# Kernel tuning notes

Measured on AMD Instinct MI355X. Metric: run time of the kernel, lower is better.

The kernel has to match this reference:

```python
import jax, jax.numpy as jnp
import numpy as np

DIM = 1024
NUM_HEADS = 16
HEAD_DIM = DIM // NUM_HEADS


def setup_inputs() -> dict:
    key = jax.random.key(0)
    k_x, k_qkv, k_proj, k_pb = jax.random.split(key, 4)
    B, N, C = 4, 2048, DIM
    x = jax.random.normal(k_x, (B, N, C), dtype=jnp.float32)
    # Dense 'qkv': kernel [C, 3C], no bias (qkv_bias=False)
    W_qkv = jax.random.normal(k_qkv, (C, 3 * C), dtype=jnp.float32) * (C ** -0.5)
    # Dense 'proj': kernel [C, C] + bias [C] (proj_bias=True)
    W_proj = jax.random.normal(k_proj, (C, C), dtype=jnp.float32) * (C ** -0.5)
    b_proj = jax.random.normal(k_pb, (C,), dtype=jnp.float32) * 0.01
    return {"x": x, "W_qkv": W_qkv, "W_proj": W_proj, "b_proj": b_proj}


def reference(x, W_qkv, W_proj, b_proj):
    B, N, C = x.shape
    H, D = NUM_HEADS, HEAD_DIM
    scale = D ** -0.5
    qkv = x @ W_qkv  # [B, N, 3C]
    qkv = qkv.reshape(B, N, 3, H, D).transpose(2, 0, 3, 1, 4)  # [3, B, H, N, D]
    q, k, v = qkv[0], qkv[1], qkv[2]
    attn = jnp.einsum('bhnd,bhmd->bhnm', q, k) * scale  # [B, H, N, N]
    attn = jax.nn.softmax(attn, axis=-1)
    out = jnp.einsum('bhnm,bhmd->bhnd', attn, v)  # [B, H, N, D]
    out = out.transpose(0, 2, 1, 3).reshape(B, N, C)
    return out @ W_proj + b_proj
```

## Files before the change

### kernel.cpp

```cpp
#include <hip/hip_runtime.h>
#include <hip/hip_bf16.h>
#include <cstdint>
#include <cstddef>

#define C_DIM 1024
#define N_HEADS 16
#define H_DIM 64
#define N_BATCH 4
#define SEQ_LEN 2048
#define N_BH 64
#define M_ROWS 8192

typedef __attribute__((ext_vector_type(8))) short bf16x8;
typedef __attribute__((ext_vector_type(4))) float f32x4;
typedef __attribute__((ext_vector_type(8))) float f32x8;
typedef __attribute__((ext_vector_type(2))) float f32x2;
typedef __attribute__((ext_vector_type(16))) float f32x16;
typedef __attribute__((ext_vector_type(4))) unsigned short us4;
typedef __attribute__((ext_vector_type(8))) unsigned short us8;
typedef __attribute__((ext_vector_type(4))) float fl4;

__device__ __forceinline__ unsigned short f2bf(float f) {
  union { float f; unsigned u; } v; v.f = f;
  unsigned r = (v.u + 0x7FFFu + ((v.u >> 16) & 1u)) >> 16;
  return (unsigned short)r;
}

__device__ __forceinline__ unsigned pk2(float a, float b) {
  union { __hip_bfloat162 h2; unsigned u; } c;
  c.h2 = __float22bfloat162_rn(float2{a, b});
  return c.u;
}

__device__ __forceinline__ void gload16(const void* g, void* l) {
  __builtin_amdgcn_global_load_lds(
      (const __attribute__((address_space(1))) unsigned int*)g,
      (__attribute__((address_space(3))) unsigned int*)l, 16, 0, 0);
}

__global__ void cast_x_kernel(const float* __restrict__ in,
                              unsigned short* __restrict__ out, int n8) {
  int i = blockIdx.x * blockDim.x + threadIdx.x;
  if (i >= n8) return;
  const fl4* p = reinterpret_cast<const fl4*>(in) + (size_t)i * 2;
  fl4 a = p[0], b = p[1];
  us8 w;
  w[0] = f2bf(a[0]); w[1] = f2bf(a[1]); w[2] = f2bf(a[2]); w[3] = f2bf(a[3]);
  w[4] = f2bf(b[0]); w[5] = f2bf(b[1]); w[6] = f2bf(b[2]); w[7] = f2bf(b[3]);
  *(reinterpret_cast<us8*>(out) + i) = w;
}

__global__ void transpose_cast_kernel(const float* __restrict__ in,
                                      unsigned short* __restrict__ out,
                                      int R, int C) {
  __shared__ float tile[64][65];
  int t = threadIdx.x;
  int tc = blockIdx.x * 64;
  int tr = blockIdx.y * 64;
  int hi = t >> 4, lo = t & 15;
#pragma unroll
  for (int i = 0; i < 4; ++i) {
    int r = i * 16 + hi;
    int c = lo * 4;
    fl4 v = *reinterpret_cast<const fl4*>(&in[(size_t)(tr + r) * C + tc + c]);
    tile[c + 0][r] = v[0]; tile[c + 1][r] = v[1];
    tile[c + 2][r] = v[2]; tile[c + 3][r] = v[3];
  }
  __syncthreads();
#pragma unroll
  for (int i = 0; i < 4; ++i) {
    int c = i * 16 + hi;
    int r = lo * 4;
    us4 w;
    w[0] = f2bf(tile[c][r + 0]); w[1] = f2bf(tile[c][r + 1]);
    w[2] = f2bf(tile[c][r + 2]); w[3] = f2bf(tile[c][r + 3]);
    *reinterpret_cast<us4*>(&out[(size_t)(tc + c) * R + tr + r]) = w;
  }
}

__global__ void transpose_v_kernel(const unsigned short* __restrict__ V,
                                   unsigned short* __restrict__ Vt) {
  __shared__ unsigned short tile[64][72];
  int t = threadIdx.x;
  int bh = blockIdx.y;
  int n0 = blockIdx.x * 64;
  const unsigned short* src = V + ((size_t)bh * SEQ_LEN + n0) * H_DIM;
#pragma unroll
  for (int i = 0; i < 2; ++i) {
    int c = t + i * 256;
    int r = c >> 3;
    int col = (c & 7) * 8;
    us8 v = *reinterpret_cast<const us8*>(&src[r * H_DIM + col]);
#pragma unroll
    for (int j = 0; j < 8; ++j) tile[col + j][r] = v[j];
  }
  __syncthreads();
  unsigned short* dst = Vt + (size_t)bh * H_DIM * SEQ_LEN + n0;
#pragma unroll
  for (int i = 0; i < 2; ++i) {
    int c = t + i * 256;
    int d = c >> 3;
    int col = (c & 7) * 8;
    us8 w;
#pragma unroll
    for (int j = 0; j < 8; ++j) w[j] = tile[d][col + j];
    *reinterpret_cast<us8*>(&dst[(size_t)d * SEQ_LEN + col]) = w;
  }
}

template <int EPI>
__global__ __launch_bounds__(256) void gemm_bt_kernel(
    const unsigned short* __restrict__ A, const unsigned short* __restrict__ Bt,
    unsigned short* __restrict__ outQ, unsigned short* __restrict__ outK,
    unsigned short* __restrict__ outV, float* __restrict__ outF,
    const float* __restrict__ bias, int K) {
  __shared__ unsigned short Alds[128 * 32];
  __shared__ unsigned short Blds[128 * 32];
  int tid = threadIdx.x;
  int lane = tid & 63, wave = tid >> 6;
  int wr = wave >> 1, wc = wave & 1;
  int brow = blockIdx.y * 128;
  int bcol = blockIdx.x * 128;
  int rr = lane & 15, g8 = (lane >> 4) * 8;

  f32x4 acc[4][4];
#pragma unroll
  for (int m = 0; m < 4; ++m)
#pragma unroll
    for (int n = 0; n < 4; ++n) acc[m][n] = (f32x4){0.f, 0.f, 0.f, 0.f};

  int c0 = tid, c1 = tid + 256;
  int r0 = c0 >> 2, o0 = (c0 & 3) * 8;
  int r1 = c1 >> 2, o1 = (c1 & 3) * 8;
  const unsigned short* Ar0 = A + (size_t)(brow + r0) * K + o0;
  const unsigned short* Ar1 = A + (size_t)(brow + r1) * K + o1;
  const unsigned short* Br0 = Bt + (size_t)(bcol + r0) * K + o0;
  const unsigned short* Br1 = Bt + (size_t)(bcol + r1) * K + o1;

  for (int k0 = 0; k0 < K; k0 += 32) {
    __syncthreads();
    gload16(Ar0 + k0, &Alds[c0 * 8]);
    gload16(Ar1 + k0, &Alds[c1 * 8]);
    gload16(Br0 + k0, &Blds[c0 * 8]);
    gload16(Br1 + k0, &Blds[c1 * 8]);
    __syncthreads();
    bf16x8 af[4], bf[4];
#pragma unroll
    for (int m = 0; m < 4; ++m)
      af[m] = *reinterpret_cast<const bf16x8*>(
          &Alds[(wr * 64 + m * 16 + rr) * 32 + g8]);
#pragma unroll
    for (int n = 0; n < 4; ++n)
      bf[n] = *reinterpret_cast<const bf16x8*>(
          &Blds[(wc * 64 + n * 16 + rr) * 32 + g8]);
#pragma unroll
    for (int m = 0; m < 4; ++m)
#pragma unroll
      for (int n = 0; n < 4; ++n)
        acc[m][n] = __builtin_amdgcn_mfma_f32_16x16x32_bf16(af[m], bf[n],
                                                            acc[m][n], 0, 0, 0);
  }

  if (EPI == 0) {
    int part = bcol >> 10;
#pragma unroll
    for (int n = 0; n < 4; ++n) {
      int col = (bcol & 1023) + wc * 64 + n * 16 + rr;
      int h = col >> 6, d = col & 63;
#pragma unroll
      for (int m = 0; m < 4; ++m) {
        int rowb = brow + wr * 64 + m * 16 + (lane >> 4) * 4;
#pragma unroll
        for (int r = 0; r < 4; ++r) {
          int mr = rowb + r;
          int b = mr >> 11, nr = mr & 2047;
          size_t idx = ((size_t)((b * N_HEADS + h) * SEQ_LEN + nr)) * H_DIM + d;
          float v = acc[m][n][r];
          if (part == 0)
            outQ[idx] = f2bf(v * 0.1803368801111837f);
          else if (part == 1)
            outK[idx] = f2bf(v);
          else
            outV[idx] = f2bf(v);
        }
      }
    }
  } else {
#pragma unroll
    for (int n = 0; n < 4; ++n) {
      int col = bcol + wc * 64 + n * 16 + rr;
      float bv = bias[col];
#pragma unroll
      for (int m = 0; m < 4; ++m) {
        int rowb = brow + wr * 64 + m * 16 + (lane >> 4) * 4;
#pragma unroll
        for (int r = 0; r < 4; ++r)
          outF[(size_t)(rowb + r) * C_DIM + col] = acc[m][n][r] + bv;
      }
    }
  }
}

__global__ __launch_bounds__(256) void attn_kernel(
    const unsigned short* __restrict__ Qs, const unsigned short* __restrict__ Ks,
    const unsigned short* __restrict__ Vts, unsigned short* __restrict__ Oo) {
  __shared__ __attribute__((aligned(16))) char lds[32768];
  const int tid = threadIdx.x;
  const int lane = tid & 63, wave = tid >> 6;
  const int l31 = lane & 31, h5 = lane >> 5;
  int i = blockIdx.x;
  int bh = (i & 7) * 8 + ((i >> 3) & 7);
  int qb = i >> 6;
  const int q0 = qb * 128 + wave * 32;
  const int bb = bh >> 4, hh = bh & 15;

  const unsigned short* Qb = Qs + (size_t)bh * SEQ_LEN * H_DIM;
  const char* Kg = (const char*)(Ks + (size_t)bh * SEQ_LEN * H_DIM);
  const char* Vg = (const char*)(Vts + (size_t)bh * H_DIM * SEQ_LEN);

  bf16x8 qf[4];
#pragma unroll
  for (int ks = 0; ks < 4; ++ks)
    qf[ks] = *reinterpret_cast<const bf16x8*>(
        &Qb[(size_t)(q0 + l31) * H_DIM + ks * 16 + h5 * 8]);

  int kaddr[4];
  int r7 = (l31 & 7) << 4;
#pragma unroll
  for (int ks = 0; ks < 4; ++ks)
    kaddr[ks] = l31 * 128 + ((ks * 32 + h5 * 16) ^ r7);
  int vaddr[2][2][2];
#pragma unroll
  for (int dt = 0; dt < 2; ++dt) {
    int d = dt * 32 + l31;
    int sw = (d & 7) << 4;
#pragma unroll
    for (int s = 0; s < 2; ++s)
#pragma unroll
      for (int m = 0; m < 2; ++m)
        vaddr[dt][s][m] = 8192 + d * 128 + ((s * 64 + m * 32 + h5 * 16) ^ sw);
  }

  const int rowc = lane >> 3;
  const int scb = (((lane & 7) ^ rowc)) * 16;
  const char* gK0 = Kg + (size_t)(wave * 16 + rowc) * 128 + scb;
  const char* gK1 = gK0 + 8 * 128;
  const char* gV0 = Vg + (size_t)(wave * 16 + rowc) * 4096 + scb;
  const char* gV1 = gV0 + 8 * 4096;
  char* lK0 = lds + wave * 2048 + (lane & 63) * 16;
  char* lV0 = lds + 8192 + wave * 2048 + (lane & 63) * 16;

  f32x16 oacc[2];
#pragma unroll
  for (int dt = 0; dt < 2; ++dt)
#pragma unroll
    for (int r = 0; r < 16; ++r) oacc[dt][r] = 0.f;
  float lsum = 0.f;

  f32x16 z16;
#pragma unroll
  for (int r = 0; r < 16; ++r) z16[r] = 0.f;

  {
    gload16(gK0, lK0);
    gload16(gK1, lK0 + 1024);
    gload16(gV0, lV0);
    gload16(gV1, lV0 + 1024);
  }
  __syncthreads();

#pragma unroll 2
  for (int t = 0; t < 32; ++t) {
    int boff = (t & 1) * 16384;
    if (t < 31) {
      int nb = ((t + 1) & 1) * 16384;
      size_t kR = (size_t)(t + 1) * 64 * 128;
      size_t kV = (size_t)(t + 1) * 128;
      gload16(gK0 + kR, lK0 + nb);
      gload16(gK1 + kR, lK0 + nb + 1024);
      gload16(gV0 + kV, lV0 + nb);
      gload16(gV1 + kV, lV0 + nb + 1024);
    }
#pragma unroll
    for (int s = 0; s < 2; ++s) {
      bf16x8 kf[4];
#pragma unroll
      for (int ks = 0; ks < 4; ++ks)
        kf[ks] = *reinterpret_cast<const bf16x8*>(
            lds + boff + kaddr[ks] + s * 4096);
      __builtin_amdgcn_s_setprio(1);
      f32x16 sa = __builtin_amdgcn_mfma_f32_32x32x16_bf16(kf[0], qf[0], z16,
                                                          0, 0, 0);
#pragma unroll
      for (int ks = 1; ks < 4; ++ks)
        sa = __builtin_amdgcn_mfma_f32_32x32x16_bf16(kf[ks], qf[ks], sa, 0, 0, 0);
      __builtin_amdgcn_s_setprio(0);
      f32x16 pv;
#pragma unroll
      for (int r = 0; r < 16; ++r) pv[r] = __builtin_amdgcn_exp2f(sa[r]);
      {
        f32x8 h8 = __builtin_shufflevector(pv, pv, 0, 1, 2, 3, 4, 5, 6, 7) +
                   __builtin_shufflevector(pv, pv, 8, 9, 10, 11, 12, 13, 14, 15);
        f32x4 h4 = __builtin_shufflevector(h8, h8, 0, 1, 2, 3) +
                   __builtin_shufflevector(h8, h8, 4, 5, 6, 7);
        f32x2 h2 = __builtin_shufflevector(h4, h4, 0, 1) +
                   __builtin_shufflevector(h4, h4, 2, 3);
        lsum += h2[0] + h2[1];
      }
      unsigned X0 = pk2(pv[0], pv[1]), X1 = pk2(pv[2], pv[3]);
      unsigned X2 = pk2(pv[4], pv[5]), X3 = pk2(pv[6], pv[7]);
      unsigned X4 = pk2(pv[8], pv[9]), X5 = pk2(pv[10], pv[11]);
      unsigned X6 = pk2(pv[12], pv[13]), X7 = pk2(pv[14], pv[15]);
      asm("v_permlane32_swap_b32 %0, %1" : "+v"(X0), "+v"(X2));
      asm("v_permlane32_swap_b32 %0, %1" : "+v"(X1), "+v"(X3));
      asm("v_permlane32_swap_b32 %0, %1" : "+v"(X4), "+v"(X6));
      asm("v_permlane32_swap_b32 %0, %1" : "+v"(X5), "+v"(X7));
      union { unsigned u[4]; bf16x8 v; } pf0, pf1;
      pf0.u[0] = X0; pf0.u[1] = X1; pf0.u[2] = X2; pf0.u[3] = X3;
      pf1.u[0] = X4; pf1.u[1] = X5; pf1.u[2] = X6; pf1.u[3] = X7;
      bf16x8 vf[2][2];
#pragma unroll
      for (int dt = 0; dt < 2; ++dt)
#pragma unroll
        for (int m = 0; m < 2; ++m)
          vf[dt][m] = *reinterpret_cast<const bf16x8*>(
              lds + boff + vaddr[dt][s][m]);
      __builtin_amdgcn_s_setprio(1);
#pragma unroll
      for (int dt = 0; dt < 2; ++dt) {
        oacc[dt] = __builtin_amdgcn_mfma_f32_32x32x16_bf16(vf[dt][0], pf0.v,
                                                           oacc[dt], 0, 0, 0);
        oacc[dt] = __builtin_amdgcn_mfma_f32_32x32x16_bf16(vf[dt][1], pf1.v,
                                                           oacc[dt], 0, 0, 0);
      }
      __builtin_amdgcn_s_setprio(0);
    }
    __syncthreads();
  }

  lsum += __shfl_xor(lsum, 32);
  float inv = 1.f / lsum;
  int n = q0 + l31;
  unsigned short* orow = Oo + ((size_t)bb * SEQ_LEN + n) * C_DIM + hh * H_DIM;
#pragma unroll
  for (int dt = 0; dt < 2; ++dt)
#pragma unroll
    for (int G = 0; G < 4; ++G) {
      us4 w;
#pragma unroll
      for (int u = 0; u < 4; ++u) w[u] = f2bf(oacc[dt][G * 4 + u] * inv);
      *reinterpret_cast<us4*>(&orow[dt * 32 + G * 8 + h5 * 4]) = w;
    }
}

extern "C" void kernel_launch(void* const* d_in, const int* in_sizes, int n_in,
                              void* d_out, int out_size, void* d_ws,
                              size_t ws_size, hipStream_t stream) {
  const float* x = (const float*)d_in[0];
  const float* Wqkv = (const float*)d_in[1];
  const float* Wproj = (const float*)d_in[2];
  const float* bproj = (const float*)d_in[3];
  float* out = (float*)d_out;

  unsigned short* xbf = (unsigned short*)d_ws;
  unsigned short* Wtqkv = xbf + (size_t)M_ROWS * C_DIM;
  unsigned short* Wtproj = Wtqkv + (size_t)3 * C_DIM * C_DIM;
  unsigned short* Qb = Wtproj + (size_t)C_DIM * C_DIM;
  unsigned short* Kb = Qb + (size_t)N_BH * SEQ_LEN * H_DIM;
  unsigned short* Vb = Kb + (size_t)N_BH * SEQ_LEN * H_DIM;
  unsigned short* Vtb = Vb + (size_t)N_BH * SEQ_LEN * H_DIM;
  unsigned short* Ob = Vb;

  cast_x_kernel<<<4096, 256, 0, stream>>>(x, xbf, M_ROWS * C_DIM / 8);
  transpose_cast_kernel<<<dim3(48, 16), 256, 0, stream>>>(Wqkv, Wtqkv, C_DIM,
                                                          3 * C_DIM);
  transpose_cast_kernel<<<dim3(16, 16), 256, 0, stream>>>(Wproj, Wtproj, C_DIM,
                                                          C_DIM);
  gemm_bt_kernel<0><<<dim3(24, 64), 256, 0, stream>>>(
      xbf, Wtqkv, Qb, Kb, Vb, nullptr, nullptr, C_DIM);
  transpose_v_kernel<<<dim3(32, 64), 256, 0, stream>>>(Vb, Vtb);
  attn_kernel<<<dim3(1024), 256, 0, stream>>>(Qb, Kb, Vtb, Ob);
  gemm_bt_kernel<1><<<dim3(8, 64), 256, 0, stream>>>(
      Ob, Wtproj, nullptr, nullptr, nullptr, out, bproj, C_DIM);
}
```

Baseline: 227.6 us.

## Triple-buffer GEMM with swizzled LDS and fuse V transpose into QKV epilogue

Rewrites the GEMM main loop to use a 3-stage LDS ring buffer with async global-to-LDS loads issued two tiles ahead, a single barrier per k-step, XOR-swizzled LDS layout to avoid bank conflicts, and raised wave priority around the MFMA block. The QKV epilogue now writes V directly in transposed layout, removing the separate transpose_v kernel and its extra pass over V. It also reuses the x buffer for the attention output. This trades more LDS per block (48KB) for fewer stalls and one fewer launch, with risk of lower occupancy and uncoalesced scattered Vt stores.

```diff
diff --git a/kernel.cpp b/kernel.cpp
--- a/kernel.cpp
+++ b/kernel.cpp
@@ -78,50 +78,36 @@
   }
 }
 
-__global__ void transpose_v_kernel(const unsigned short* __restrict__ V,
-                                   unsigned short* __restrict__ Vt) {
-  __shared__ unsigned short tile[64][72];
-  int t = threadIdx.x;
-  int bh = blockIdx.y;
-  int n0 = blockIdx.x * 64;
-  const unsigned short* src = V + ((size_t)bh * SEQ_LEN + n0) * H_DIM;
-#pragma unroll
-  for (int i = 0; i < 2; ++i) {
-    int c = t + i * 256;
-    int r = c >> 3;
-    int col = (c & 7) * 8;
-    us8 v = *reinterpret_cast<const us8*>(&src[r * H_DIM + col]);
-#pragma unroll
-    for (int j = 0; j < 8; ++j) tile[col + j][r] = v[j];
-  }
-  __syncthreads();
-  unsigned short* dst = Vt + (size_t)bh * H_DIM * SEQ_LEN + n0;
-#pragma unroll
-  for (int i = 0; i < 2; ++i) {
-    int c = t + i * 256;
-    int d = c >> 3;
-    int col = (c & 7) * 8;
-    us8 w;
-#pragma unroll
-    for (int j = 0; j < 8; ++j) w[j] = tile[d][col + j];
-    *reinterpret_cast<us8*>(&dst[(size_t)d * SEQ_LEN + col]) = w;
-  }
-}
-
 template <int EPI>
-__global__ __launch_bounds__(256) void gemm_bt_kernel(
+__global__ __launch_bounds__(256, 3) void gemm_v2_kernel(
     const unsigned short* __restrict__ A, const unsigned short* __restrict__ Bt,
     unsigned short* __restrict__ outQ, unsigned short* __restrict__ outK,
-    unsigned short* __restrict__ outV, float* __restrict__ outF,
+    unsigned short* __restrict__ outVt, float* __restrict__ outF,
     const float* __restrict__ bias, int K) {
-  __shared__ unsigned short Alds[128 * 32];
-  __shared__ unsigned short Blds[128 * 32];
-  int tid = threadIdx.x;
-  int lane = tid & 63, wave = tid >> 6;
-  int wr = wave >> 1, wc = wave & 1;
-  int brow = blockIdx.y * 128;
-  int bcol = blockIdx.x * 128;
-  int rr = lane & 15, g8 = (lane >> 4) * 8;
+  __shared__ __attribute__((aligned(16))) char lds[3 * 16384];
+  const int tid = threadIdx.x;
+  const int lane = tid & 63, wave = tid >> 6;
+  const int wr = wave >> 1, wn = wave & 1;
+  const int brow = blockIdx.y * 128;
+  const int bcol = blockIdx.x * 128;
+  const int rr = lane & 15, g = lane >> 4;
+
+  const int rbase =
+      (rr >> 1) * 128 + (((((rr & 1) << 2) | g) ^ (rr >> 1)) << 4);
+
+  const int s1 = tid + 256;
+  const int l0 = tid >> 3, v0 = (tid & 7) ^ (l0 & 7);
+  const int l1 = s1 >> 3, v1 = (s1 & 7) ^ (l1 & 7);
+  const int m0 = 2 * l0 + (v0 >> 2), g0 = v0 & 3;
+  const int m1 = 2 * l1 + (v1 >> 2), g1 = v1 & 3;
+  const char* srcA0 = (const char*)(A + (size_t)(brow + m0) * K + g0 * 8);
+  const char* srcA1 = (const char*)(A + (size_t)(brow + m1) * K + g1 * 8);
+  const char* srcB0 = (const char*)(Bt + (size_t)(bcol + m0) * K + g0 * 8);
+  const char* srcB1 = (const char*)(Bt + (size_t)(bcol + m1) * K + g1 * 8);
+  const int oA0 = wave * 1024 + (lane & 63) * 16;
+  const int oA1 = oA0 + 4096;
+  const int oB0 = oA0 + 8192;
+  const int oB1 = oA0 + 12288;
 
   f32x4 acc[4][4];
 #pragma unroll
@@ -129,73 +115,102 @@
 #pragma unroll
     for (int n = 0; n < 4; ++n) acc[m][n] = (f32x4){0.f, 0.f, 0.f, 0.f};
 
-  int c0 = tid, c1 = tid + 256;
-  int r0 = c0 >> 2, o0 = (c0 & 3) * 8;
-  int r1 = c1 >> 2, o1 = (c1 & 3) * 8;
-  const unsigned short* Ar0 = A + (size_t)(brow + r0) * K + o0;
-  const unsigned short* Ar1 = A + (size_t)(brow + r1) * K + o1;
-  const unsigned short* Br0 = Bt + (size_t)(bcol + r0) * K + o0;
-  const unsigned short* Br1 = Bt + (size_t)(bcol + r1) * K + o1;
-
-  for (int k0 = 0; k0 < K; k0 += 32) {
-    __syncthreads();
-    gload16(Ar0 + k0, &Alds[c0 * 8]);
-    gload16(Ar1 + k0, &Alds[c1 * 8]);
-    gload16(Br0 + k0, &Blds[c0 * 8]);
-    gload16(Br1 + k0, &Blds[c1 * 8]);
-    __syncthreads();
+  const int NT = K >> 5;
+
+#pragma unroll
+  for (int pt = 0; pt < 2; ++pt) {
+    char* bb = lds + pt * 16384;
+    size_t ko = (size_t)pt * 64;
+    gload16(srcA0 + ko, bb + oA0);
+    gload16(srcA1 + ko, bb + oA1);
+    gload16(srcB0 + ko, bb + oB0);
+    gload16(srcB1 + ko, bb + oB1);
+  }
+
+  int rbuf = 0, nbuf = 2;
+  for (int kt = 0; kt < NT; ++kt) {
+    if (kt < NT - 1) {
+      asm volatile("s_waitcnt vmcnt(4)" ::: "memory");
+    } else {
+      asm volatile("s_waitcnt vmcnt(0)" ::: "memory");
+    }
+    __builtin_amdgcn_sched_barrier(0);
+    __builtin_amdgcn_s_barrier();
+    __builtin_amdgcn_sched_barrier(0);
+    if (kt + 2 < NT) {
+      char* bb = lds + nbuf * 16384;
+      size_t ko = (size_t)(kt + 2) * 64;
+      gload16(srcA0 + ko, bb + oA0);
+      gload16(srcA1 + ko, bb + oA1);
+      gload16(srcB0 + ko, bb + oB0);
+      gload16(srcB1 + ko, bb + oB1);
+    }
+    const char* rb = lds + rbuf * 16384;
     bf16x8 af[4], bf[4];
 #pragma unroll
-    for (int m = 0; m < 4; ++m)
-      af[m] = *reinterpret_cast<const bf16x8*>(
-          &Alds[(wr * 64 + m * 16 + rr) * 32 + g8]);
-#pragma unroll
-    for (int n = 0; n < 4; ++n)
-      bf[n] = *reinterpret_cast<const bf16x8*>(
-          &Blds[(wc * 64 + n * 16 + rr) * 32 + g8]);
-#pragma unroll
-    for (int m = 0; m < 4; ++m)
-#pragma unroll
-      for (int n = 0; n < 4; ++n)
-        acc[m][n] = __builtin_amdgcn_mfma_f32_16x16x32_bf16(af[m], bf[n],
-                                                            acc[m][n], 0, 0, 0);
+    for (int fm = 0; fm < 4; ++fm)
+      af[fm] = *reinterpret_cast<const bf16x8*>(rb + wr * 4096 + fm * 1024 +
+                                                rbase);
+#pragma unroll
+    for (int fn = 0; fn < 4; ++fn)
+      bf[fn] = *reinterpret_cast<const bf16x8*>(rb + 8192 + wn * 4096 +
+                                                fn * 1024 + rbase);
+    asm volatile("s_waitcnt lgkmcnt(0)" ::: "memory");
+    __builtin_amdgcn_sched_barrier(0);
+    __builtin_amdgcn_s_setprio(1);
+#pragma unroll
+    for (int fm = 0; fm < 4; ++fm)
+#pragma unroll
+      for (int fn = 0; fn < 4; ++fn)
+        acc[fm][fn] = __builtin_amdgcn_mfma_f32_16x16x32_bf16(
+            af[fm], bf[fn], acc[fm][fn], 0, 0, 0);
+    __builtin_amdgcn_s_setprio(0);
+    rbuf = rbuf == 2 ? 0 : rbuf + 1;
+    nbuf = nbuf == 2 ? 0 : nbuf + 1;
   }
 
   if (EPI == 0) {
     int part = bcol >> 10;
 #pragma unroll
-    for (int n = 0; n < 4; ++n) {
-      int col = (bcol & 1023) + wc * 64 + n * 16 + rr;
+    for (int fn = 0; fn < 4; ++fn) {
+      int col = (bcol & 1023) + wn * 64 + fn * 16 + rr;
       int h = col >> 6, d = col & 63;
 #pragma unroll
-      for (int m = 0; m < 4; ++m) {
-        int rowb = brow + wr * 64 + m * 16 + (lane >> 4) * 4;
-#pragma unroll
-        for (int r = 0; r < 4; ++r) {
-          int mr = rowb + r;
-          int b = mr >> 11, nr = mr & 2047;
-          size_t idx = ((size_t)((b * N_HEADS + h) * SEQ_LEN + nr)) * H_DIM + d;
-          float v = acc[m][n][r];
-          if (part == 0)
-            outQ[idx] = f2bf(v * 0.1803368801111837f);
-          else if (part == 1)
-            outK[idx] = f2bf(v);
-          else
-            outV[idx] = f2bf(v);
+      for (int fm = 0; fm < 4; ++fm) {
+        int rowb = brow + wr * 64 + fm * 16 + g * 4;
+        int b = rowb >> 11, nr = rowb & 2047;
+        if (part == 2) {
+          us4 w;
+#pragma unroll
+          for (int r = 0; r < 4; ++r) w[r] = f2bf(acc[fm][fn][r]);
+          *reinterpret_cast<us4*>(
+              &outVt[((size_t)((b * N_HEADS + h) * H_DIM + d)) * SEQ_LEN +
+                     nr]) = w;
+        } else {
+#pragma unroll
+          for (int r = 0; r < 4; ++r) {
+            size_t idx =
+                ((size_t)((b * N_HEADS + h) * SEQ_LEN + nr + r)) * H_DIM + d;
+            float v = acc[fm][fn][r];
+            if (part == 0)
+              outQ[idx] = f2bf(v * 0.1803368801111837f);
+            else
+              outK[idx] = f2bf(v);
+          }
         }
       }
     }
   } else {
 #pragma unroll
-    for (int n = 0; n < 4; ++n) {
-      int col = bcol + wc * 64 + n * 16 + rr;
+    for (int fn = 0; fn < 4; ++fn) {
+      int col = bcol + wn * 64 + fn * 16 + rr;
       float bv = bias[col];
 #pragma unroll
-      for (int m = 0; m < 4; ++m) {
-        int rowb = brow + wr * 64 + m * 16 + (lane >> 4) * 4;
+      for (int fm = 0; fm < 4; ++fm) {
+        int rowb = brow + wr * 64 + fm * 16 + g * 4;
 #pragma unroll
         for (int r = 0; r < 4; ++r)
-          outF[(size_t)(rowb + r) * C_DIM + col] = acc[m][n][r] + bv;
+          outF[(size_t)(rowb + r) * C_DIM + col] = acc[fm][fn][r] + bv;
       }
     }
   }
@@ -367,19 +382,17 @@
   unsigned short* Wtproj = Wtqkv + (size_t)3 * C_DIM * C_DIM;
   unsigned short* Qb = Wtproj + (size_t)C_DIM * C_DIM;
   unsigned short* Kb = Qb + (size_t)N_BH * SEQ_LEN * H_DIM;
-  unsigned short* Vb = Kb + (size_t)N_BH * SEQ_LEN * H_DIM;
-  unsigned short* Vtb = Vb + (size_t)N_BH * SEQ_LEN * H_DIM;
-  unsigned short* Ob = Vb;
+  unsigned short* Vtb = Kb + (size_t)N_BH * SEQ_LEN * H_DIM;
+  unsigned short* Ob = xbf;
 
   cast_x_kernel<<<4096, 256, 0, stream>>>(x, xbf, M_ROWS * C_DIM / 8);
   transpose_cast_kernel<<<dim3(48, 16), 256, 0, stream>>>(Wqkv, Wtqkv, C_DIM,
                                                           3 * C_DIM);
   transpose_cast_kernel<<<dim3(16, 16), 256, 0, stream>>>(Wproj, Wtproj, C_DIM,
                                                           C_DIM);
-  gemm_bt_kernel<0><<<dim3(24, 64), 256, 0, stream>>>(
-      xbf, Wtqkv, Qb, Kb, Vb, nullptr, nullptr, C_DIM);
-  transpose_v_kernel<<<dim3(32, 64), 256, 0, stream>>>(Vb, Vtb);
+  gemm_v2_kernel<0><<<dim3(24, 64), 256, 0, stream>>>(
+      xbf, Wtqkv, Qb, Kb, Vtb, nullptr, nullptr, C_DIM);
   attn_kernel<<<dim3(1024), 256, 0, stream>>>(Qb, Kb, Vtb, Ob);
-  gemm_bt_kernel<1><<<dim3(8, 64), 256, 0, stream>>>(
+  gemm_v2_kernel<1><<<dim3(8, 64), 256, 0, stream>>>(
       Ob, Wtproj, nullptr, nullptr, nullptr, out, bproj, C_DIM);
 }
```

New measurement: 208.4 us. 8.5% less time.
